# Performance work log

Hardware: AMD Instinct MI355X
Metric: run time of the kernel (lower is better)

Reference implementation:

```python
import jax, jax.numpy as jnp
import numpy as np

N_NODES = 50000
N_EDGES = 800000
N_GRAPHS = 500
IN_DIM, HID, OUT = 128, 64, 10


def setup_inputs() -> dict:
    key = jax.random.key(0)
    ks = jax.random.split(key, 12)
    x = jax.random.normal(ks[0], (N_NODES, IN_DIM), dtype=jnp.float32)
    edge_index = jax.random.randint(ks[1], (2, N_EDGES), 0, N_NODES, dtype=jnp.int32)
    batch = jnp.sort(jax.random.randint(ks[2], (N_NODES,), 0, N_GRAPHS, dtype=jnp.int32))
    def glorot(k, shape):
        lim = np.sqrt(6.0 / (shape[0] + shape[1]))
        return jax.random.uniform(k, shape, jnp.float32, -lim, lim)
    return {
        "x": x, "edge_index": edge_index, "batch": batch,
        "W1": glorot(ks[3], (IN_DIM, HID)), "b1": jnp.zeros((HID,), jnp.float32),
        "W2": glorot(ks[4], (HID, HID)),    "b2": jnp.zeros((HID,), jnp.float32),
        "W3": glorot(ks[5], (HID, HID)),    "b3": jnp.zeros((HID,), jnp.float32),
        "lin_W1": glorot(ks[6], (HID, HID)), "lin_b1": jnp.zeros((HID,), jnp.float32),
        "lin_W2": glorot(ks[7], (HID, OUT)), "lin_b2": jnp.zeros((OUT,), jnp.float32),
    }


def _gcn_conv(x, src, dst, deg_inv_sqrt, W, b):
    # PyG GCNConv: h = x @ W, then sym-normalized scatter-add over edges (self-loops included in src/dst)
    h = x @ W                                   # [N, out]
    norm = deg_inv_sqrt[src] * deg_inv_sqrt[dst]  # [E+N]
    msgs = h[src] * norm[:, None]               # [E+N, out]  (large gathered intermediate)
    out = jax.ops.segment_sum(msgs, dst, num_segments=N_NODES)
    return out + b


def reference(x, edge_index, batch, W1, b1, W2, b2, W3, b3, lin_W1, lin_b1, lin_W2, lin_b2):
    # add self-loops once; degree (with edge weight 1) computed on target nodes
    loops = jnp.arange(N_NODES, dtype=edge_index.dtype)
    src = jnp.concatenate([edge_index[0], loops])
    dst = jnp.concatenate([edge_index[1], loops])
    deg = jax.ops.segment_sum(jnp.ones_like(dst, dtype=x.dtype), dst, num_segments=N_NODES)
    deg_inv_sqrt = jnp.where(deg > 0, jax.lax.rsqrt(jnp.maximum(deg, 1e-12)), 0.0)

    h = jax.nn.relu(_gcn_conv(x, src, dst, deg_inv_sqrt, W1, b1))
    h = jax.nn.relu(_gcn_conv(h, src, dst, deg_inv_sqrt, W2, b2))
    h = jax.nn.relu(_gcn_conv(h, src, dst, deg_inv_sqrt, W3, b3))

    # global mean pool over graphs
    sums = jax.ops.segment_sum(h, batch, num_segments=N_GRAPHS)
    counts = jax.ops.segment_sum(jnp.ones((h.shape[0],), h.dtype), batch, num_segments=N_GRAPHS)
    pooled = sums / jnp.maximum(counts, 1.0)[:, None]  # [G, HID]

    # MLP head (dropout p=0 / eval -> identity)
    logits = jax.nn.relu(pooled @ lin_W1 + lin_b1) @ lin_W2 + lin_b2
    return (logits, jnp.zeros((), x.dtype))
```

## Files before the change

kernel.cpp:

```cpp
#include <hip/hip_runtime.h>
#include <hip/hip_bf16.h>

#define N_NODES 50000
#define N_EDGES 800000
#define N_GRAPHS 500
#define IN_DIM 128
#define HID 64
#define OUT_DIM 10
#define NB_BUCK ((N_NODES + 63) >> 6)
#define NBLK 256
#define BLDT 1024

__device__ __forceinline__ float bf2f(unsigned short u) {
    return __uint_as_float(((unsigned)u) << 16);
}
__device__ __forceinline__ unsigned short f2bf(float f) {
    unsigned x = __float_as_uint(f);
    x += 0x7fffu + ((x >> 16) & 1u);
    return (unsigned short)(x >> 16);
}
__device__ __forceinline__ void acc8(float a[8], uint4 r) {
    a[0] += __uint_as_float(r.x << 16);
    a[1] += __uint_as_float(r.x & 0xffff0000u);
    a[2] += __uint_as_float(r.y << 16);
    a[3] += __uint_as_float(r.y & 0xffff0000u);
    a[4] += __uint_as_float(r.z << 16);
    a[5] += __uint_as_float(r.z & 0xffff0000u);
    a[6] += __uint_as_float(r.w << 16);
    a[7] += __uint_as_float(r.w & 0xffff0000u);
}

__device__ __forceinline__ void gather_node(const unsigned short* __restrict__ hs,
                                            const int* __restrict__ csr_src,
                                            int node, int beg, int end, int f8, float a[8]) {
    {
        uint4 u = *(const uint4*)&hs[(size_t)node * 64 + f8];
        acc8(a, u);
    }
    int j = beg;
    for (; j + 7 < end; j += 8) {
        int s0 = csr_src[j];
        int s1 = csr_src[j + 1];
        int s2 = csr_src[j + 2];
        int s3 = csr_src[j + 3];
        int s4 = csr_src[j + 4];
        int s5 = csr_src[j + 5];
        int s6 = csr_src[j + 6];
        int s7 = csr_src[j + 7];
        uint4 r0 = *(const uint4*)&hs[(size_t)s0 * 64 + f8];
        uint4 r1 = *(const uint4*)&hs[(size_t)s1 * 64 + f8];
        uint4 r2 = *(const uint4*)&hs[(size_t)s2 * 64 + f8];
        uint4 r3 = *(const uint4*)&hs[(size_t)s3 * 64 + f8];
        uint4 r4 = *(const uint4*)&hs[(size_t)s4 * 64 + f8];
        uint4 r5 = *(const uint4*)&hs[(size_t)s5 * 64 + f8];
        uint4 r6 = *(const uint4*)&hs[(size_t)s6 * 64 + f8];
        uint4 r7 = *(const uint4*)&hs[(size_t)s7 * 64 + f8];
        acc8(a, r0); acc8(a, r1); acc8(a, r2); acc8(a, r3);
        acc8(a, r4); acc8(a, r5); acc8(a, r6); acc8(a, r7);
    }
    if (j + 3 < end) {
        int s0 = csr_src[j];
        int s1 = csr_src[j + 1];
        int s2 = csr_src[j + 2];
        int s3 = csr_src[j + 3];
        uint4 r0 = *(const uint4*)&hs[(size_t)s0 * 64 + f8];
        uint4 r1 = *(const uint4*)&hs[(size_t)s1 * 64 + f8];
        uint4 r2 = *(const uint4*)&hs[(size_t)s2 * 64 + f8];
        uint4 r3 = *(const uint4*)&hs[(size_t)s3 * 64 + f8];
        acc8(a, r0); acc8(a, r1); acc8(a, r2); acc8(a, r3);
        j += 4;
    }
    if (j + 1 < end) {
        int s0 = csr_src[j];
        int s1 = csr_src[j + 1];
        uint4 r0 = *(const uint4*)&hs[(size_t)s0 * 64 + f8];
        uint4 r1 = *(const uint4*)&hs[(size_t)s1 * 64 + f8];
        acc8(a, r0); acc8(a, r1);
        j += 2;
    }
    if (j < end) {
        int s0 = csr_src[j];
        uint4 r0 = *(const uint4*)&hs[(size_t)s0 * 64 + f8];
        acc8(a, r0);
    }
}

__global__ __launch_bounds__(BLDT) void p1_hist_kernel(const int* __restrict__ dst,
                                                       int* __restrict__ bhist,
                                                       float* __restrict__ gsum,
                                                       int e, int epb) {
    __shared__ int h[NB_BUCK];
    int tid = threadIdx.x;
    int blk = blockIdx.x;
    {
        int z = blk * BLDT + tid;
        if (z < N_GRAPHS * HID) gsum[z] = 0.0f;
    }
    for (int i = tid; i < NB_BUCK; i += BLDT) h[i] = 0;
    __syncthreads();
    int e0 = blk * epb;
    int e1 = e0 + epb;
    if (e1 > e) e1 = e;
    int i = e0 + tid * 4;
    for (; i + 3 < e1; i += BLDT * 4) {
        int4 d4 = *(const int4*)&dst[i];
        atomicAdd(&h[d4.x >> 6], 1);
        atomicAdd(&h[d4.y >> 6], 1);
        atomicAdd(&h[d4.z >> 6], 1);
        atomicAdd(&h[d4.w >> 6], 1);
    }
    for (int k = i; k < e1 && k < i + 4; ++k) atomicAdd(&h[dst[k] >> 6], 1);
    __syncthreads();
    for (int j = tid; j < NB_BUCK; j += BLDT) bhist[blk * NB_BUCK + j] = h[j];
}

__global__ __launch_bounds__(NBLK) void scanA_kernel(int* __restrict__ bhist,
                                                     int* __restrict__ bsum) {
    __shared__ int s[NBLK];
    int b = blockIdx.x;
    int t = threadIdx.x;
    int c = bhist[t * NB_BUCK + b];
    s[t] = c;
    __syncthreads();
    for (int off = 1; off < NBLK; off <<= 1) {
        int x = (t >= off) ? s[t - off] : 0;
        __syncthreads();
        s[t] += x;
        __syncthreads();
    }
    bhist[t * NB_BUCK + b] = s[t] - c;
    if (t == NBLK - 1) bsum[b] = s[t];
}

__global__ __launch_bounds__(BLDT) void p2_place_kernel(
    const int* __restrict__ src, const int* __restrict__ dst,
    const int* __restrict__ bsum, const int* __restrict__ base,
    unsigned* __restrict__ pairs, int* __restrict__ bstart, int e, int epb) {
    __shared__ int h[NB_BUCK];
    __shared__ int sb[NB_BUCK];
    __shared__ int ts[BLDT];
    int tid = threadIdx.x;
    int blk = blockIdx.x;
    int i0 = tid << 2;
    int v0 = 0, v1 = 0, v2 = 0, v3 = 0;
    if (i0 < NB_BUCK) v0 = bsum[i0];
    if (i0 + 1 < NB_BUCK) v1 = bsum[i0 + 1];
    if (i0 + 2 < NB_BUCK) v2 = bsum[i0 + 2];
    if (i0 + 3 < NB_BUCK) v3 = bsum[i0 + 3];
    int tsum = v0 + v1 + v2 + v3;
    ts[tid] = tsum;
    for (int i = tid; i < NB_BUCK; i += BLDT) h[i] = 0;
    __syncthreads();
    for (int off = 1; off < BLDT; off <<= 1) {
        int x = (tid >= off) ? ts[tid - off] : 0;
        __syncthreads();
        ts[tid] += x;
        __syncthreads();
    }
    int excl = ts[tid] - tsum;
    int s0 = excl;
    int s1 = s0 + v0;
    int s2 = s1 + v1;
    int s3 = s2 + v2;
    const int* bb = base + blk * NB_BUCK;
    if (i0 < NB_BUCK) sb[i0] = s0 + bb[i0];
    if (i0 + 1 < NB_BUCK) sb[i0 + 1] = s1 + bb[i0 + 1];
    if (i0 + 2 < NB_BUCK) sb[i0 + 2] = s2 + bb[i0 + 2];
    if (i0 + 3 < NB_BUCK) sb[i0 + 3] = s3 + bb[i0 + 3];
    if (blk == 0) {
        if (i0 < NB_BUCK) bstart[i0] = s0;
        if (i0 + 1 < NB_BUCK) bstart[i0 + 1] = s1;
        if (i0 + 2 < NB_BUCK) bstart[i0 + 2] = s2;
        if (i0 + 3 < NB_BUCK) bstart[i0 + 3] = s3;
        if (tid == 0) bstart[NB_BUCK] = e;
    }
    __syncthreads();
    int e0 = blk * epb;
    int e1 = e0 + epb;
    if (e1 > e) e1 = e;
    int i = e0 + tid * 4;
    for (; i + 3 < e1; i += BLDT * 4) {
        int4 d4 = *(const int4*)&dst[i];
        int4 s4 = *(const int4*)&src[i];
        int b0 = d4.x >> 6, b1 = d4.y >> 6, b2 = d4.z >> 6, b3 = d4.w >> 6;
        int r0 = atomicAdd(&h[b0], 1);
        int r1 = atomicAdd(&h[b1], 1);
        int r2 = atomicAdd(&h[b2], 1);
        int r3 = atomicAdd(&h[b3], 1);
        pairs[sb[b0] + r0] = ((unsigned)(d4.x & 63) << 16) | (unsigned)s4.x;
        pairs[sb[b1] + r1] = ((unsigned)(d4.y & 63) << 16) | (unsigned)s4.y;
        pairs[sb[b2] + r2] = ((unsigned)(d4.z & 63) << 16) | (unsigned)s4.z;
        pairs[sb[b3] + r3] = ((unsigned)(d4.w & 63) << 16) | (unsigned)s4.w;
    }
    for (int k = i; k < e1 && k < i + 4; ++k) {
        int d = dst[k];
        int b = d >> 6;
        int r = atomicAdd(&h[b], 1);
        pairs[sb[b] + r] = ((unsigned)(d & 63) << 16) | (unsigned)src[k];
    }
}

__global__ __launch_bounds__(256) void csr_lin1_kernel(
    const unsigned* __restrict__ pairs, const int* __restrict__ bstart,
    int* __restrict__ rs, float* __restrict__ dinv, int* __restrict__ csr_src,
    const float* __restrict__ A, const float* __restrict__ W,
    unsigned short* __restrict__ C, int n) {
    const int K = IN_DIM;
    __shared__ float As[64][K + 4];
    __shared__ float Ws[K][64];
    __shared__ int lcnt[64];
    __shared__ int lcur[64];
    __shared__ float sdinv[64];
    int b = blockIdx.x;
    int tid = threadIdx.x;
    int beg = bstart[b], end = bstart[b + 1];
    if (tid < 64) lcnt[tid] = 0;
    __syncthreads();
    for (int i = beg + tid; i < end; i += 256) atomicAdd(&lcnt[pairs[i] >> 16], 1);
    __syncthreads();
    if (tid < 64) {
        int c = lcnt[tid];
        int v = c;
#pragma unroll
        for (int off = 1; off < 64; off <<= 1) {
            int t = __shfl_up(v, off);
            if (tid >= off) v += t;
        }
        int excl = v - c;
        int node = b * 64 + tid;
        float dv = rsqrtf((float)(c + 1));
        if (node <= n) {
            rs[node] = beg + excl;
            if (node < n) dinv[node] = dv;
        }
        sdinv[tid] = dv;
        lcur[tid] = beg + excl;
    }
    __syncthreads();
    for (int i = beg + tid; i < end; i += 256) {
        unsigned p = pairs[i];
        int slot = atomicAdd(&lcur[p >> 16], 1);
        csr_src[slot] = (int)(p & 0xffffu);
    }

    int block0 = b * 64;
    int rows = n - block0;
    if (rows > 64) rows = 64;

    const float* Abase = A + (size_t)block0 * K;
    int totalA4 = (rows * K) >> 2;
    for (int i4 = tid; i4 < totalA4; i4 += 256) {
        int i = i4 << 2;
        float4 v = *(const float4*)(Abase + i);
        *(float4*)&As[i / K][i % K] = v;
    }
    {
        const float4* Wv = (const float4*)W;
        float4* Wsv = (float4*)&Ws[0][0];
        for (int i = tid; i < K * 16; i += 256) Wsv[i] = Wv[i];
    }
    __syncthreads();

    int tx = tid & 15;
    int ty = tid >> 4;
    float acc[4][4] = {};
#pragma unroll 2
    for (int k = 0; k < K; k += 4) {
        float4 a[4];
#pragma unroll
        for (int i = 0; i < 4; ++i) a[i] = *(const float4*)&As[ty * 4 + i][k];
        float4 w[4];
#pragma unroll
        for (int kk = 0; kk < 4; ++kk) w[kk] = *(const float4*)&Ws[k + kk][tx * 4];
#pragma unroll
        for (int i = 0; i < 4; ++i) {
            float av[4] = {a[i].x, a[i].y, a[i].z, a[i].w};
#pragma unroll
            for (int kk = 0; kk < 4; ++kk) {
                acc[i][0] += av[kk] * w[kk].x;
                acc[i][1] += av[kk] * w[kk].y;
                acc[i][2] += av[kk] * w[kk].z;
                acc[i][3] += av[kk] * w[kk].w;
            }
        }
    }

#pragma unroll
    for (int i = 0; i < 4; ++i) {
        int r = ty * 4 + i;
        if (r < rows) {
            float s = sdinv[r];
            ushort4 v;
            v.x = f2bf(acc[i][0] * s);
            v.y = f2bf(acc[i][1] * s);
            v.z = f2bf(acc[i][2] * s);
            v.w = f2bf(acc[i][3] * s);
            *(ushort4*)&C[(size_t)(block0 + r) * 64 + tx * 4] = v;
        }
    }
}

__global__ __launch_bounds__(256) void gather_lin_kernel(
    const unsigned short* __restrict__ hs, const int* __restrict__ rs,
    const int* __restrict__ csr_src, const float* __restrict__ dinv,
    const float* __restrict__ bias, const float* __restrict__ W,
    unsigned short* __restrict__ C, int n) {
    const int K = HID;
    __shared__ float As[32][K + 4];
    __shared__ float Ws[K][64];
    int tid = threadIdx.x;
    int block0 = blockIdx.x * 32;
    int rows = n - block0;
    if (rows > 32) rows = 32;

    {
        const float4* Wv = (const float4*)W;
        float4* Wsv = (float4*)&Ws[0][0];
        for (int i = tid; i < K * 16; i += 256) Wsv[i] = Wv[i];
    }

    int grp = tid >> 3;
    int lg = tid & 7;
    int f8 = lg << 3;
    float4 bb0 = *(const float4*)&bias[f8];
    float4 bb1 = *(const float4*)&bias[f8 + 4];

    int node = block0 + grp;
    float a[8] = {0.f, 0.f, 0.f, 0.f, 0.f, 0.f, 0.f, 0.f};
    if (node < n) {
        int beg = rs[node], end = rs[node + 1];
        gather_node(hs, csr_src, node, beg, end, f8, a);
        float sc = dinv[node];
        a[0] = fmaxf(a[0] * sc + bb0.x, 0.f);
        a[1] = fmaxf(a[1] * sc + bb0.y, 0.f);
        a[2] = fmaxf(a[2] * sc + bb0.z, 0.f);
        a[3] = fmaxf(a[3] * sc + bb0.w, 0.f);
        a[4] = fmaxf(a[4] * sc + bb1.x, 0.f);
        a[5] = fmaxf(a[5] * sc + bb1.y, 0.f);
        a[6] = fmaxf(a[6] * sc + bb1.z, 0.f);
        a[7] = fmaxf(a[7] * sc + bb1.w, 0.f);
    }
    {
        float4 w0 = {a[0], a[1], a[2], a[3]};
        float4 w1 = {a[4], a[5], a[6], a[7]};
        *(float4*)&As[grp][f8] = w0;
        *(float4*)&As[grp][f8 + 4] = w1;
    }
    __syncthreads();

    int tx = tid & 15;
    int ty = tid >> 4;
    float acc[2][4] = {};
#pragma unroll 2
    for (int k = 0; k < K; k += 4) {
        float4 aa[2];
#pragma unroll
        for (int i = 0; i < 2; ++i) aa[i] = *(const float4*)&As[ty * 2 + i][k];
        float4 w[4];
#pragma unroll
        for (int kk = 0; kk < 4; ++kk) w[kk] = *(const float4*)&Ws[k + kk][tx * 4];
#pragma unroll
        for (int i = 0; i < 2; ++i) {
            float av[4] = {aa[i].x, aa[i].y, aa[i].z, aa[i].w};
#pragma unroll
            for (int kk = 0; kk < 4; ++kk) {
                acc[i][0] += av[kk] * w[kk].x;
                acc[i][1] += av[kk] * w[kk].y;
                acc[i][2] += av[kk] * w[kk].z;
                acc[i][3] += av[kk] * w[kk].w;
            }
        }
    }

#pragma unroll
    for (int i = 0; i < 2; ++i) {
        int r = ty * 2 + i;
        if (r < rows) {
            float s = dinv[block0 + r];
            ushort4 v;
            v.x = f2bf(acc[i][0] * s);
            v.y = f2bf(acc[i][1] * s);
            v.z = f2bf(acc[i][2] * s);
            v.w = f2bf(acc[i][3] * s);
            *(ushort4*)&C[(size_t)(block0 + r) * 64 + tx * 4] = v;
        }
    }
}

__global__ __launch_bounds__(256) void gather_pool_kernel(
    const unsigned short* __restrict__ hs, const int* __restrict__ rs,
    const int* __restrict__ csr_src, const float* __restrict__ dinv,
    const float* __restrict__ bias, const int* __restrict__ batch,
    float* __restrict__ gsum, int n) {
    __shared__ float As[32][68];
    int tid = threadIdx.x;
    int block0 = blockIdx.x * 32;
    int rows = n - block0;
    if (rows > 32) rows = 32;

    int grp = tid >> 3;
    int lg = tid & 7;
    int f8 = lg << 3;
    float4 bb0 = *(const float4*)&bias[f8];
    float4 bb1 = *(const float4*)&bias[f8 + 4];

    int node = block0 + grp;
    float a[8] = {0.f, 0.f, 0.f, 0.f, 0.f, 0.f, 0.f, 0.f};
    if (node < n) {
        int beg = rs[node], end = rs[node + 1];
        gather_node(hs, csr_src, node, beg, end, f8, a);
        float sc = dinv[node];
        a[0] = fmaxf(a[0] * sc + bb0.x, 0.f);
        a[1] = fmaxf(a[1] * sc + bb0.y, 0.f);
        a[2] = fmaxf(a[2] * sc + bb0.z, 0.f);
        a[3] = fmaxf(a[3] * sc + bb0.w, 0.f);
        a[4] = fmaxf(a[4] * sc + bb1.x, 0.f);
        a[5] = fmaxf(a[5] * sc + bb1.y, 0.f);
        a[6] = fmaxf(a[6] * sc + bb1.z, 0.f);
        a[7] = fmaxf(a[7] * sc + bb1.w, 0.f);
    }
    {
        float4 w0 = {a[0], a[1], a[2], a[3]};
        float4 w1 = {a[4], a[5], a[6], a[7]};
        *(float4*)&As[grp][f8] = w0;
        *(float4*)&As[grp][f8 + 4] = w1;
    }
    __syncthreads();

    int q = tid >> 6;
    int f = tid & 63;
    int r0 = q * 8;
    int r1 = r0 + 8;
    if (r1 > rows) r1 = rows;
    if (r0 < rows) {
        int gprev = batch[block0 + r0];
        float run = 0.0f;
        for (int r = r0; r < r1; ++r) {
            int g = batch[block0 + r];
            if (g != gprev) {
                atomicAdd(&gsum[(size_t)gprev * 64 + f], run);
                run = 0.0f;
                gprev = g;
            }
            run += As[r][f];
        }
        atomicAdd(&gsum[(size_t)gprev * 64 + f], run);
    }
}

__device__ __forceinline__ int lower_bound_dev(const int* __restrict__ a, int n, int v) {
    int lo = 0, hi = n;
    while (lo < hi) {
        int m = (lo + hi) >> 1;
        if (a[m] < v) lo = m + 1; else hi = m;
    }
    return lo;
}

__global__ __launch_bounds__(64) void head_kernel(
    const float* __restrict__ gsum, const int* __restrict__ batch,
    const float* __restrict__ W1, const float* __restrict__ b1,
    const float* __restrict__ W2, const float* __restrict__ b2,
    float* __restrict__ out, int nNodes, int nGraphs) {
    __shared__ float p[64];
    __shared__ float t64[64];
    int g = blockIdx.x;
    int f = threadIdx.x;
    int lo = lower_bound_dev(batch, nNodes, g);
    int hi = lower_bound_dev(batch, nNodes, g + 1);
    float inv = 1.0f / fmaxf((float)(hi - lo), 1.0f);
    p[f] = gsum[(size_t)g * 64 + f] * inv;
    __syncthreads();
    float acc = b1[f];
#pragma unroll
    for (int k = 0; k < 64; ++k) acc += p[k] * W1[k * 64 + f];
    t64[f] = fmaxf(acc, 0.0f);
    __syncthreads();
    if (f < OUT_DIM) {
        float acc2 = b2[f];
#pragma unroll
        for (int k = 0; k < 64; ++k) acc2 += t64[k] * W2[k * OUT_DIM + f];
        out[g * OUT_DIM + f] = acc2;
    }
    if (g == 0 && f == 0) out[nGraphs * OUT_DIM] = 0.0f;
}

extern "C" void kernel_launch(void* const* d_in, const int* in_sizes, int n_in,
                              void* d_out, int out_size, void* d_ws, size_t ws_size,
                              hipStream_t stream) {
    const float* x      = (const float*)d_in[0];
    const int*   eidx   = (const int*)d_in[1];
    const int*   batch  = (const int*)d_in[2];
    const float* W1     = (const float*)d_in[3];
    const float* b1     = (const float*)d_in[4];
    const float* W2     = (const float*)d_in[5];
    const float* b2     = (const float*)d_in[6];
    const float* W3     = (const float*)d_in[7];
    const float* b3     = (const float*)d_in[8];
    const float* lin_W1 = (const float*)d_in[9];
    const float* lin_b1 = (const float*)d_in[10];
    const float* lin_W2 = (const float*)d_in[11];
    const float* lin_b2 = (const float*)d_in[12];
    float* out = (float*)d_out;

    const int E = in_sizes[1] / 2;
    const int N = N_NODES;
    const int NF = N * HID;
    int epb = (E + NBLK - 1) / NBLK;
    epb = (epb + 7) & ~7;

    const int* src = eidx;
    const int* dst = eidx + E;

    unsigned short* buf1 = (unsigned short*)d_ws;
    unsigned short* buf2 = buf1 + NF;
    float* dinv = (float*)(buf2 + NF);
    int* bhist  = (int*)(dinv + N);
    int* bsum   = bhist + NBLK * NB_BUCK;
    int* bstart = bsum + NB_BUCK;
    int* rs     = bstart + NB_BUCK + 1;
    int* csr_src = rs + N + 1;
    unsigned* pairs = (unsigned*)(csr_src + E);
    float* gsum = (float*)(pairs + E);

    const int TILES = (N + 63) / 64;
    const int G32 = (N + 31) / 32;

    p1_hist_kernel<<<NBLK, BLDT, 0, stream>>>(dst, bhist, gsum, E, epb);
    scanA_kernel<<<NB_BUCK, NBLK, 0, stream>>>(bhist, bsum);
    p2_place_kernel<<<NBLK, BLDT, 0, stream>>>(src, dst, bsum, bhist, pairs, bstart, E, epb);

    csr_lin1_kernel<<<TILES, 256, 0, stream>>>(pairs, bstart, rs, dinv, csr_src,
                                               x, W1, buf1, N);

    gather_lin_kernel<<<G32, 256, 0, stream>>>(buf1, rs, csr_src, dinv, b1, W2, buf2, N);

    gather_lin_kernel<<<G32, 256, 0, stream>>>(buf2, rs, csr_src, dinv, b2, W3, buf1, N);

    gather_pool_kernel<<<G32, 256, 0, stream>>>(buf1, rs, csr_src, dinv, b3, batch, gsum, N);

    head_kernel<<<N_GRAPHS, 64, 0, stream>>>(gsum, batch, lin_W1, lin_b1, lin_W2, lin_b2,
                                             out, N, N_GRAPHS);
}
```

Before: 205.5 us.

## Split weight tiles in K halves to cut LDS and raise occupancy

```diff
diff --git a/kernel.cpp b/kernel.cpp
--- a/kernel.cpp
+++ b/kernel.cpp
@@ -11,9 +11,6 @@
 #define NBLK 256
 #define BLDT 1024
 
-__device__ __forceinline__ float bf2f(unsigned short u) {
-    return __uint_as_float(((unsigned)u) << 16);
-}
 __device__ __forceinline__ unsigned short f2bf(float f) {
     unsigned x = __float_as_uint(f);
     x += 0x7fffu + ((x >> 16) & 1u);
@@ -200,14 +197,13 @@
     }
 }
 
-__global__ __launch_bounds__(256) void csr_lin1_kernel(
+__global__ __launch_bounds__(256, 4) void csr_lin1_kernel(
     const unsigned* __restrict__ pairs, const int* __restrict__ bstart,
     int* __restrict__ rs, float* __restrict__ dinv, int* __restrict__ csr_src,
     const float* __restrict__ A, const float* __restrict__ W,
     unsigned short* __restrict__ C, int n) {
-    const int K = IN_DIM;
-    __shared__ float As[64][K + 4];
-    __shared__ float Ws[K][64];
+    __shared__ float As[64][68];
+    __shared__ float Ws[64][64];
     __shared__ int lcnt[64];
     __shared__ int lcur[64];
     __shared__ float sdinv[64];
@@ -246,41 +242,44 @@
     int block0 = b * 64;
     int rows = n - block0;
     if (rows > 64) rows = 64;
-
-    const float* Abase = A + (size_t)block0 * K;
-    int totalA4 = (rows * K) >> 2;
-    for (int i4 = tid; i4 < totalA4; i4 += 256) {
-        int i = i4 << 2;
-        float4 v = *(const float4*)(Abase + i);
-        *(float4*)&As[i / K][i % K] = v;
-    }
-    {
-        const float4* Wv = (const float4*)W;
-        float4* Wsv = (float4*)&Ws[0][0];
-        for (int i = tid; i < K * 16; i += 256) Wsv[i] = Wv[i];
-    }
-    __syncthreads();
-
     int tx = tid & 15;
     int ty = tid >> 4;
     float acc[4][4] = {};
+
+    for (int half = 0; half < 2; ++half) {
+        __syncthreads();
+        {
+            const float4* Wv = (const float4*)(W + half * 64 * HID);
+            float4* Wsv = (float4*)&Ws[0][0];
+            for (int i = tid; i < 64 * 16; i += 256) Wsv[i] = Wv[i];
+        }
+        for (int idx = tid; idx < 64 * 16; idx += 256) {
+            int r = idx >> 4;
+            int c4 = (idx & 15) << 2;
+            float4 v = {0.f, 0.f, 0.f, 0.f};
+            if (r < rows)
+                v = *(const float4*)&A[(size_t)(block0 + r) * IN_DIM + half * 64 + c4];
+            *(float4*)&As[r][c4] = v;
+        }
+        __syncthreads();
 #pragma unroll 2
-    for (int k = 0; k < K; k += 4) {
-        float4 a[4];
-#pragma unroll
-        for (int i = 0; i < 4; ++i) a[i] = *(const float4*)&As[ty * 4 + i][k];
-        float4 w[4];
-#pragma unroll
-        for (int kk = 0; kk < 4; ++kk) w[kk] = *(const float4*)&Ws[k + kk][tx * 4];
-#pragma unroll
-        for (int i = 0; i < 4; ++i) {
-            float av[4] = {a[i].x, a[i].y, a[i].z, a[i].w};
-#pragma unroll
-            for (int kk = 0; kk < 4; ++kk) {
-                acc[i][0] += av[kk] * w[kk].x;
-                acc[i][1] += av[kk] * w[kk].y;
-                acc[i][2] += av[kk] * w[kk].z;
-                acc[i][3] += av[kk] * w[kk].w;
+        for (int k = 0; k < 64; k += 4) {
+            float4 a[4];
+#pragma unroll
+            for (int i = 0; i < 4; ++i) a[i] = *(const float4*)&As[ty * 4 + i][k];
+            float4 w[4];
+#pragma unroll
+            for (int kk = 0; kk < 4; ++kk) w[kk] = *(const float4*)&Ws[k + kk][tx * 4];
+#pragma unroll
+            for (int i = 0; i < 4; ++i) {
+                float av[4] = {a[i].x, a[i].y, a[i].z, a[i].w};
+#pragma unroll
+                for (int kk = 0; kk < 4; ++kk) {
+                    acc[i][0] += av[kk] * w[kk].x;
+                    acc[i][1] += av[kk] * w[kk].y;
+                    acc[i][2] += av[kk] * w[kk].z;
+                    acc[i][3] += av[kk] * w[kk].w;
+                }
             }
         }
     }
@@ -300,14 +299,13 @@
     }
 }
 
-__global__ __launch_bounds__(256) void gather_lin_kernel(
+__global__ __launch_bounds__(256, 8) void gather_lin_kernel(
     const unsigned short* __restrict__ hs, const int* __restrict__ rs,
     const int* __restrict__ csr_src, const float* __restrict__ dinv,
     const float* __restrict__ bias, const float* __restrict__ W,
     unsigned short* __restrict__ C, int n) {
-    const int K = HID;
-    __shared__ float As[32][K + 4];
-    __shared__ float Ws[K][64];
+    __shared__ float As[32][68];
+    __shared__ float Ws[32][64];
     int tid = threadIdx.x;
     int block0 = blockIdx.x * 32;
     int rows = n - block0;
@@ -316,7 +314,7 @@
     {
         const float4* Wv = (const float4*)W;
         float4* Wsv = (float4*)&Ws[0][0];
-        for (int i = tid; i < K * 16; i += 256) Wsv[i] = Wv[i];
+        for (int i = tid; i < 32 * 16; i += 256) Wsv[i] = Wv[i];
     }
 
     int grp = tid >> 3;
@@ -350,12 +348,39 @@
 
     int tx = tid & 15;
     int ty = tid >> 4;
-    float acc[2][4] = {};
+    float acc[2][4] = {{0.f, 0.f, 0.f, 0.f}, {0.f, 0.f, 0.f, 0.f}};
 #pragma unroll 2
-    for (int k = 0; k < K; k += 4) {
+    for (int k = 0; k < 32; k += 4) {
         float4 aa[2];
 #pragma unroll
         for (int i = 0; i < 2; ++i) aa[i] = *(const float4*)&As[ty * 2 + i][k];
+        float4 w[4];
+#pragma unroll
+        for (int kk = 0; kk < 4; ++kk) w[kk] = *(const float4*)&Ws[k + kk][tx * 4];
+#pragma unroll
+        for (int i = 0; i < 2; ++i) {
+            float av[4] = {aa[i].x, aa[i].y, aa[i].z, aa[i].w};
+#pragma unroll
+            for (int kk = 0; kk < 4; ++kk) {
+                acc[i][0] += av[kk] * w[kk].x;
+                acc[i][1] += av[kk] * w[kk].y;
+                acc[i][2] += av[kk] * w[kk].z;
+                acc[i][3] += av[kk] * w[kk].w;
+            }
+        }
+    }
+    __syncthreads();
+    {
+        const float4* Wv = (const float4*)(W + 32 * HID);
+        float4* Wsv = (float4*)&Ws[0][0];
+        for (int i = tid; i < 32 * 16; i += 256) Wsv[i] = Wv[i];
+    }
+    __syncthreads();
+#pragma unroll 2
+    for (int k = 0; k < 32; k += 4) {
+        float4 aa[2];
+#pragma unroll
+        for (int i = 0; i < 2; ++i) aa[i] = *(const float4*)&As[ty * 2 + i][32 + k];
         float4 w[4];
 #pragma unroll
         for (int kk = 0; kk < 4; ++kk) w[kk] = *(const float4*)&Ws[k + kk][tx * 4];
@@ -387,7 +412,7 @@
     }
 }
 
-__global__ __launch_bounds__(256) void gather_pool_kernel(
+__global__ __launch_bounds__(256, 8) void gather_pool_kernel(
     const unsigned short* __restrict__ hs, const int* __restrict__ rs,
     const int* __restrict__ csr_src, const float* __restrict__ dinv,
     const float* __restrict__ bias, const int* __restrict__ batch,
```

New measurement: 252.2 us. 1.23x slower.
